# Kernel optimization log

Measured on AMD Instinct MI355X. Metric: run time of the kernel, lower is better.

Reference implementation:

```python
import jax, jax.numpy as jnp
import numpy as np

TAU = 0.5
EPS = 1e-6
RAY_STEPS = 128
N_SECANT = 8
STEPS_IN = 64
STEPS_OUT = 32
RADIUS = 1.0
ADA_START, ADA_END, ADA_DECAY = 2.0, 0.1, 1.5e-5
IT = 100000
DEPTH_NEAR = 0.0
DELTA = float(max(ADA_START * np.exp(-ADA_DECAY * IT), ADA_END))


def _occ_val(p, W1, b1, W2, b2):
    # occupancy probability minus tau (sign change = surface crossing)
    h = jax.nn.softplus(p @ W1 + b1)
    return jax.nn.sigmoid((h @ W2 + b2)[..., 0]) - TAU


def _rgb_alpha(p, v, W1, b1, W2, b2, Wc1, bc1, Wc2, bc2):
    alpha = _occ_val(p, W1, b1, W2, b2) + TAU
    f = jax.nn.relu(jnp.concatenate([p, v], -1) @ Wc1 + bc1)
    rgb = jax.nn.sigmoid(f @ Wc2 + bc2)
    return rgb, alpha


def _forward(pixels, camera_mat, world_mat, scale_mat, W1, b1, W2, b2, Wc1, bc1, Wc2, bc2):
    B, N, _ = pixels.shape
    # transform_to_world with all matrices inverted: p_world = S^-1 W^-1 C^-1 p_hom
    M = jnp.linalg.inv(scale_mat) @ jnp.linalg.inv(world_mat) @ jnp.linalg.inv(camera_mat)
    ones = jnp.ones((B, N, 1), pixels.dtype)
    p_h = jnp.concatenate([pixels, ones, ones], -1)  # (x, y, 1, 1) with depth 1
    pixels_world = jnp.einsum('bij,bnj->bni', M, p_h)[..., :3]
    origin = jnp.array([0.0, 0.0, 0.0, 1.0], pixels.dtype)
    cam0 = jnp.einsum('bij,j->bi', M, origin)[..., :3]                 # (B,3)
    camera_world = jnp.broadcast_to(cam0[:, None, :], (B, N, 3))
    ray = pixels_world - camera_world
    ray = ray / jnp.linalg.norm(ray, axis=-1, keepdims=True)

    # ---- sphere intersection ----
    rcd = jnp.einsum('bnd,bd->bn', ray, cam0)
    under = rcd ** 2 - (jnp.sum(cam0 ** 2, -1)[:, None] - RADIUS ** 2)
    mask_int = under > 0
    s = jnp.sqrt(jnp.where(mask_int, under, 1.0))                      # safe sqrt
    inters = jnp.stack([-s - rcd, s - rcd], -1)
    inters = jnp.where(mask_int[..., None], inters, 0.0)
    inters = jnp.maximum(inters, 0.0)                                  # (B,N,2)
    d_far = inters[..., 1]

    # ---- ray marching + secant root finding (no grad in original) ----
    t = jnp.linspace(0.0, 1.0, RAY_STEPS, dtype=pixels.dtype)
    d_prop = d_far[..., None] * t                                      # (B,N,S)
    p_prop = camera_world[:, :, None, :] + ray[:, :, None, :] * d_prop[..., None]
    val = _occ_val(p_prop, W1, b1, W2, b2)                             # (B,N,S)
    mask_0_free = val[..., 0] < 0
    sign = jnp.sign(val[..., :-1] * val[..., 1:])
    sign = jnp.concatenate([sign, jnp.ones_like(sign[..., :1])], -1)
    cost = sign * jnp.arange(RAY_STEPS, 0, -1, dtype=pixels.dtype)
    ind = jnp.argmin(cost, -1)
    mask_sc = jnp.min(cost, -1) < 0
    f_low = jnp.take_along_axis(val, ind[..., None], -1)[..., 0]
    mask = mask_sc & (f_low < 0) & mask_int & mask_0_free
    ind_hi = jnp.minimum(ind + 1, RAY_STEPS - 1)
    d_low = jnp.take_along_axis(d_prop, ind[..., None], -1)[..., 0]
    d_high = jnp.take_along_axis(d_prop, ind_hi[..., None], -1)[..., 0]
    f_high = jnp.take_along_axis(val, ind_hi[..., None], -1)[..., 0]

    def sec(f_l, f_h, d_l, d_h):
        den = f_h - f_l
        return jnp.where(jnp.abs(den) > 1e-12, -f_l * (d_h - d_l) / den + d_l, 0.5 * (d_l + d_h))

    def body(i, c):
        d_p, d_l, f_l, d_h, f_h = c
        f_m = _occ_val(camera_world + ray * d_p[..., None], W1, b1, W2, b2)
        low = f_m < 0
        d_l = jnp.where(low, d_p, d_l); f_l = jnp.where(low, f_m, f_l)
        d_h = jnp.where(low, d_h, d_p); f_h = jnp.where(low, f_h, f_m)
        return (sec(f_l, f_h, d_l, d_h), d_l, f_l, d_h, f_h)

    d_pred0 = sec(f_low, f_high, d_low, d_high)
    d_pred, _, _, _, _ = jax.lax.fori_loop(0, N_SECANT, body, (d_pred0, d_low, f_low, d_high, f_high))
    d_i = jnp.where(mask, d_pred, jnp.inf)
    d_i = jnp.where(mask_0_free, d_i, 0.0)
    d_i = jax.lax.stop_gradient(d_i)

    # ---- depth interval selection ----
    mask_zero = d_i == 0
    mask_pred = jnp.isfinite(d_i)
    dists = jnp.where(mask_pred, d_i, 1.0)
    dists = jnp.where(mask_zero, 0.0, dists)[0]                        # batch 1, as original
    obj_mask = (mask_pred & ~mask_zero)[0]                             # (N,)
    cam_f = camera_world.reshape(-1, 3)
    ray_f = ray.reshape(-1, 3)
    d_surf = inters.reshape(-1, 2)[:, 1]
    dnp = jnp.maximum(dists - DELTA, DEPTH_NEAR)
    dfp = jnp.minimum(dists + DELTA, d_surf)
    FULL = STEPS_IN + STEPS_OUT
    t_full = jnp.linspace(0.0, 1.0, FULL, dtype=pixels.dtype)
    d_bg = d_surf[:, None] * t_full                                    # depth_range[0] = 0
    t_in = jnp.linspace(0.0, 1.0, STEPS_IN, dtype=pixels.dtype)
    t_out = jnp.linspace(0.0, 1.0, STEPS_OUT, dtype=pixels.dtype)
    d_in = dnp[:, None] * (1.0 - t_in) + dfp[:, None] * t_in
    d_out = dnp[:, None] * t_out
    d_obj = jnp.sort(jnp.concatenate([d_out, d_in], -1), -1)
    d_all = jnp.where(obj_mask[:, None], d_obj, d_bg)                  # (N, FULL)

    # ---- shading + alpha compositing ----
    p_fg = cam_f[:, None, :] + ray_f[:, None, :] * d_all[..., None]    # (N,FULL,3)
    v_fg = jnp.broadcast_to(-ray_f[:, None, :], p_fg.shape)
    rgb, alpha = _rgb_alpha(p_fg, v_fg, W1, b1, W2, b2, Wc1, bc1, Wc2, bc2)
    trans = jnp.cumprod(jnp.concatenate([jnp.ones_like(alpha[:, :1]), 1.0 - alpha + EPS], -1), -1)[:, :-1]
    w = alpha * trans
    rgb_values = jnp.sum(w[..., None] * rgb, -2)
    return rgb_values.reshape(B, N, 3)


def setup_inputs() -> dict:
    key = jax.random.key(0)
    ks = jax.random.split(key, 8)
    B, N, H = 1, 4096, 128
    pixels = jax.random.uniform(ks[0], (B, N, 2), minval=-1.0, maxval=1.0, dtype=jnp.float32)
    camera_mat = jnp.broadcast_to(jnp.diag(jnp.array([2.0, 2.0, 1.0, 1.0], jnp.float32)), (B, 4, 4))
    world_mat = jnp.broadcast_to(jnp.array([[1, 0, 0, 0], [0, 1, 0, 0], [0, 0, 1, 2.0], [0, 0, 0, 1]], jnp.float32), (B, 4, 4))
    scale_mat = jnp.broadcast_to(jnp.eye(4, dtype=jnp.float32), (B, 4, 4))
    W1 = jax.random.normal(ks[1], (3, H), jnp.float32)
    b1 = 0.1 * jax.random.normal(ks[2], (H,), jnp.float32)
    W2 = 0.5 * jax.random.normal(ks[3], (H, 1), jnp.float32)
    b2 = jnp.zeros((1,), jnp.float32)
    Wc1 = 0.5 * jax.random.normal(ks[4], (6, H), jnp.float32)
    bc1 = jnp.zeros((H,), jnp.float32)
    Wc2 = 0.5 * jax.random.normal(ks[5], (H, 3), jnp.float32)
    bc2 = jnp.zeros((3,), jnp.float32)
    return dict(pixels=pixels, camera_mat=camera_mat, world_mat=world_mat, scale_mat=scale_mat,
                W1=W1, b1=b1, W2=W2, b2=b2, Wc1=Wc1, bc1=bc1, Wc2=Wc2, bc2=bc2)


def reference(pixels, camera_mat, world_mat, scale_mat, W1, b1, W2, b2, Wc1, bc1, Wc2, bc2):
    return _forward(pixels, camera_mat, world_mat, scale_mat, W1, b1, W2, b2, Wc1, bc1, Wc2, bc2)
```

## Files before the change

kernel.cpp:

```cpp
#include <hip/hip_runtime.h>
#include <math.h>


namespace {

constexpr int H_    = 128;
constexpr int RS    = 128;
constexpr int NSEC  = 8;
constexpr int SOUT_ = 32;
constexpr int SIN_  = 64;
constexpr int FULL_ = 96;
constexpr float EPSA   = 1e-6f;
constexpr float DELTA_ = 0.44626032029685964f;
constexpr float L2E    = 1.4426950408889634f;
constexpr float LN2    = 0.6931471805599453f;

typedef __attribute__((ext_vector_type(2))) float f2;

__device__ __forceinline__ f2 s2(float v) { return f2{v, v}; }

constexpr float PC0 =  0.5849625007211562f;
constexpr float PC1 =  0.4808983469629878f;
constexpr float PC2 = -0.0801497244938313f;
constexpr float PC3 =  0.0178110498875181f;
constexpr float PC4 = -0.0044527624718795f;
constexpr float PC5 =  0.0011873633258345f;
constexpr float PC6 = -0.0003298231460651f;

__device__ __forceinline__ f2 sp2p(f2 u) {
    f2 e;
    e.x = __builtin_amdgcn_exp2f(-fabsf(u.x));
    e.y = __builtin_amdgcn_exp2f(-fabsf(u.y));
    f2 t = e + e - 1.0f;
    f2 p = s2(PC6);
    p = __builtin_elementwise_fma(p, t, s2(PC5));
    p = __builtin_elementwise_fma(p, t, s2(PC4));
    p = __builtin_elementwise_fma(p, t, s2(PC3));
    p = __builtin_elementwise_fma(p, t, s2(PC2));
    p = __builtin_elementwise_fma(p, t, s2(PC1));
    p = __builtin_elementwise_fma(p, t, s2(PC0));
    return __builtin_elementwise_max(u, s2(0.0f)) + p;
}

__device__ __forceinline__ float sigmoid_fast(float x) {
    return __builtin_amdgcn_rcpf(1.0f + __expf(-x));
}
__device__ __forceinline__ float sgnf(float p) {
    return (p > 0.0f) ? 1.0f : ((p < 0.0f) ? -1.0f : 0.0f);
}
__device__ __forceinline__ float secant_step(float f_l, float f_h, float d_l, float d_h) {
    float den = f_h - f_l;
    if (fabsf(den) > 1e-12f) return -f_l * (d_h - d_l) / den + d_l;
    return 0.5f * (d_l + d_h);
}

__device__ void inv4(const float* m, float* o) {
    float inv[16];
    inv[0]  =  m[5]*m[10]*m[15] - m[5]*m[11]*m[14] - m[9]*m[6]*m[15] + m[9]*m[7]*m[14] + m[13]*m[6]*m[11] - m[13]*m[7]*m[10];
    inv[4]  = -m[4]*m[10]*m[15] + m[4]*m[11]*m[14] + m[8]*m[6]*m[15] - m[8]*m[7]*m[14] - m[12]*m[6]*m[11] + m[12]*m[7]*m[10];
    inv[8]  =  m[4]*m[9]*m[15]  - m[4]*m[11]*m[13] - m[8]*m[5]*m[15] + m[8]*m[7]*m[13] + m[12]*m[5]*m[11] - m[12]*m[7]*m[9];
    inv[12] = -m[4]*m[9]*m[14]  + m[4]*m[10]*m[13] + m[8]*m[5]*m[14] - m[8]*m[6]*m[13] - m[12]*m[5]*m[10] + m[12]*m[6]*m[9];
    inv[1]  = -m[1]*m[10]*m[15] + m[1]*m[11]*m[14] + m[9]*m[2]*m[15] - m[9]*m[3]*m[14] - m[13]*m[2]*m[11] + m[13]*m[3]*m[10];
    inv[5]  =  m[0]*m[10]*m[15] - m[0]*m[11]*m[14] - m[8]*m[2]*m[15] + m[8]*m[3]*m[14] + m[12]*m[2]*m[11] - m[12]*m[3]*m[10];
    inv[9]  = -m[0]*m[9]*m[15]  + m[0]*m[11]*m[13] + m[8]*m[1]*m[15] - m[8]*m[3]*m[13] - m[12]*m[1]*m[11] + m[12]*m[3]*m[9];
    inv[13] =  m[0]*m[9]*m[14]  - m[0]*m[10]*m[13] - m[8]*m[1]*m[14] + m[8]*m[2]*m[13] + m[12]*m[1]*m[10] - m[12]*m[2]*m[9];
    inv[2]  =  m[1]*m[6]*m[15]  - m[1]*m[7]*m[14]  - m[5]*m[2]*m[15] + m[5]*m[3]*m[14] + m[13]*m[2]*m[7]  - m[13]*m[3]*m[6];
    inv[6]  = -m[0]*m[6]*m[15]  + m[0]*m[7]*m[14]  + m[4]*m[2]*m[15] - m[4]*m[3]*m[14] - m[12]*m[2]*m[7]  + m[12]*m[3]*m[6];
    inv[10] =  m[0]*m[5]*m[15]  - m[0]*m[7]*m[13]  - m[4]*m[1]*m[15] + m[4]*m[3]*m[13] + m[12]*m[1]*m[7]  - m[12]*m[3]*m[5];
    inv[14] = -m[0]*m[5]*m[14]  + m[0]*m[6]*m[13]  + m[4]*m[1]*m[14] - m[4]*m[2]*m[13] - m[12]*m[1]*m[6]  + m[12]*m[2]*m[5];
    inv[3]  = -m[1]*m[6]*m[11]  + m[1]*m[7]*m[10]  + m[5]*m[2]*m[11] - m[5]*m[3]*m[10] - m[9]*m[2]*m[7]   + m[9]*m[3]*m[6];
    inv[7]  =  m[0]*m[6]*m[11]  - m[0]*m[7]*m[10]  - m[4]*m[2]*m[11] + m[4]*m[3]*m[10] + m[8]*m[2]*m[7]   - m[8]*m[3]*m[6];
    inv[11] = -m[0]*m[5]*m[11]  + m[0]*m[7]*m[9]   + m[4]*m[1]*m[11] - m[4]*m[3]*m[9]  - m[8]*m[1]*m[7]   + m[8]*m[3]*m[5];
    inv[15] =  m[0]*m[5]*m[10]  - m[0]*m[6]*m[9]   - m[4]*m[1]*m[10] + m[4]*m[2]*m[9]  + m[8]*m[1]*m[6]   - m[8]*m[2]*m[5];
    float det = m[0]*inv[0] + m[1]*inv[4] + m[2]*inv[8] + m[3]*inv[12];
    float idet = 1.0f / det;
    for (int i = 0; i < 16; i++) o[i] = inv[i] * idet;
}

__global__ __launch_bounds__(64) void render_k(
    const float* __restrict__ pixels,
    const float* __restrict__ Cm, const float* __restrict__ Wm, const float* __restrict__ Sm,
    const float* __restrict__ W1, const float* __restrict__ b1,
    const float* __restrict__ W2, const float* __restrict__ b2,
    const float* __restrict__ Wc1, const float* __restrict__ bc1,
    const float* __restrict__ Wc2, const float* __restrict__ bc2,
    float* __restrict__ out, int N)
{
    const int tid = threadIdx.x;
    const int r   = blockIdx.x;

    __shared__ float4 sP0[H_/2];
    __shared__ float4 sP1[H_/2];
    __shared__ float4 sP2[H_/2];
    __shared__ float4 sP3[H_/2];
    __shared__ f2     sW2[H_/2];
    __shared__ float  sInv[3][16];
    __shared__ float  sT[16], sM[16];

    {
        const float* mm = (tid == 0) ? Cm : ((tid == 1) ? Wm : Sm);
        float o[16];
        inv4(mm, o);
        if (tid < 3)
            for (int k = 0; k < 16; k++) sInv[tid][k] = o[k];
    }
    __syncthreads();
    if (tid < 16) {
        int row = tid >> 2, col = tid & 3;
        float s = 0.0f;
        for (int k = 0; k < 4; k++) s += sInv[1][row*4 + k] * sInv[0][k*4 + col];
        sT[tid] = s;
    }
    __syncthreads();
    if (tid < 16) {
        int row = tid >> 2, col = tid & 3;
        float s = 0.0f;
        for (int k = 0; k < 4; k++) s += sInv[2][row*4 + k] * sT[k*4 + col];
        sM[tid] = s;
    }
    __syncthreads();

    float cx, cy, cz, rx, ry, rz, dfar;
    int mint;
    {
        const float px_ = pixels[2*r], py_ = pixels[2*r + 1];
        float cam[3], dir[3];
        for (int i = 0; i < 3; i++) {
            cam[i] = sM[4*i + 3];
            float pw = sM[4*i + 0]*px_ + sM[4*i + 1]*py_ + sM[4*i + 2] + sM[4*i + 3];
            dir[i] = pw - cam[i];
        }
        float nrm = sqrtf(dir[0]*dir[0] + dir[1]*dir[1] + dir[2]*dir[2]);
        rx = dir[0]/nrm; ry = dir[1]/nrm; rz = dir[2]/nrm;
        cx = cam[0]; cy = cam[1]; cz = cam[2];
        float rcd = rx*cx + ry*cy + rz*cz;
        float cc  = cx*cx + cy*cy + cz*cz;
        float under = rcd*rcd - (cc - 1.0f);
        mint = under > 0.0f;
        float s = sqrtf(mint ? under : 1.0f);
        dfar = mint ? fmaxf(s - rcd, 0.0f) : 0.0f;
    }

    float a2k[2], c2k[2], w2k[2];
    float cCr[2], w0r[2], w1r[2], w2r[2];
#pragma unroll
    for (int k = 0; k < 2; k++) {
        const int u = 2*tid + k;
        float w1x = W1[u], w1y = W1[H_ + u], w1z = W1[2*H_ + u];
        float b1j = b1[u], w2j = W2[u];
        a2k[k] = (w1x*rx + w1y*ry + w1z*rz) * L2E;
        c2k[k] = (w1x*cx + w1y*cy + w1z*cz + b1j) * L2E;
        w2k[k] = w2j * LN2;
        float q0 = Wc1[u],        q1 = Wc1[H_ + u],  q2 = Wc1[2*H_ + u];
        float q3 = Wc1[3*H_ + u], q4 = Wc1[4*H_ + u], q5 = Wc1[5*H_ + u];
        float aC = q0*rx + q1*ry + q2*rz;
        cCr[k] = q0*cx + q1*cy + q2*cz + bc1[u] - (q3*rx + q4*ry + q5*rz);
        w0r[k] = Wc2[3*u + 0]; w1r[k] = Wc2[3*u + 1]; w2r[k] = Wc2[3*u + 2];
        if (k == 0) {
            sP0[tid].x = a2k[0]; sP0[tid].z = c2k[0];
            sP1[tid].x = w2k[0]; sP1[tid].z = aC;
            sP2[tid].x = cCr[0]; sP2[tid].z = w0r[0];
            sP3[tid].x = w1r[0]; sP3[tid].z = w2r[0];
        } else {
            sP0[tid].y = a2k[1]; sP0[tid].w = c2k[1];
            sP1[tid].y = w2k[1]; sP1[tid].w = aC;
            sP2[tid].y = cCr[1]; sP2[tid].w = w0r[1];
            sP3[tid].y = w1r[1]; sP3[tid].w = w2r[1];
        }
    }
    sW2[tid] = f2{w2k[0], w2k[1]};
    const float b2v  = b2[0];
    const float bc20 = bc2[0], bc21 = bc2[1], bc22 = bc2[2];
    __syncthreads();

    float alpha0, r0c, g0c, b0c;
    float alpha1, r1c, g1c, b1c;

    if (dfar == 0.0f) {
        f2 sp = sp2p(f2{c2k[0], c2k[1]});
        float part = sp.x*w2k[0] + sp.y*w2k[1];
        f2 ff = __builtin_elementwise_max(f2{cCr[0], cCr[1]}, s2(0.0f));
        float A0 = ff.x*w0r[0] + ff.y*w0r[1];
        float A1 = ff.x*w1r[0] + ff.y*w1r[1];
        float A2 = ff.x*w2r[0] + ff.y*w2r[1];
#pragma unroll
        for (int off = 32; off; off >>= 1) {
            part += __shfl_xor(part, off, 64);
            A0   += __shfl_xor(A0,   off, 64);
            A1   += __shfl_xor(A1,   off, 64);
            A2   += __shfl_xor(A2,   off, 64);
        }
        alpha0 = sigmoid_fast(part + b2v);
        r0c = sigmoid_fast(A0 + bc20);
        g0c = sigmoid_fast(A1 + bc21);
        b0c = sigmoid_fast(A2 + bc22);
        alpha1 = alpha0; r1c = r0c; g1c = g0c; b1c = b0c;
    } else {
        const float inv127 = 1.0f / (RS - 1);

        float l0;
        {
            f2 sp = sp2p(f2{c2k[0], c2k[1]});
            float part = sp.x*w2k[0] + sp.y*w2k[1];
#pragma unroll
            for (int off = 32; off; off >>= 1) part += __shfl_xor(part, off, 64);
            l0 = part + b2v;
        }

        float d_i;
        if (l0 >= 0.0f) {
            d_i = 0.0f;
        } else {
            auto march_logit = [&](float dsmp) -> float {
                const f2 dd = s2(dsmp);
                f2 acc = s2(0.0f);
#pragma unroll 4
                for (int j2 = 0; j2 < H_/2; j2++) {
                    float4 q0 = sP0[j2];
                    f2 wv = sW2[j2];
                    f2 u = __builtin_elementwise_fma(f2{q0.x, q0.y}, dd, f2{q0.z, q0.w});
                    acc = __builtin_elementwise_fma(sp2p(u), wv, acc);
                }
                return acc.x + acc.y + b2v;
            };

            float lA = march_logit(dfar * ((float)tid * inv127));
            float va = sigmoid_fast(lA) - 0.5f;
            float van = __shfl_down(va, 1, 64);
            float ca = (tid < 63) ? sgnf(va * van) * (float)(RS - tid) : 1.0f;
            float cmin = ca; int ind = tid;
#pragma unroll
            for (int off = 32; off; off >>= 1) {
                float c2 = __shfl_xor(cmin, off, 64);
                int   i2 = __shfl_xor(ind,  off, 64);
                if (c2 < cmin || (c2 == cmin && i2 < ind)) { cmin = c2; ind = i2; }
            }
            int crossed = cmin < 0.0f;
            float f_low = 0.0f, f_high = 0.0f;
            if (crossed) {
                f_low  = __shfl(va, ind, 64);
                f_high = __shfl(va, ind + 1, 64);
            } else {
                float lB = march_logit(dfar * ((float)(tid + 64) * inv127));
                float vb = sigmoid_fast(lB) - 0.5f;
                float v63 = __shfl(va, 63, 64);
                float v64 = __shfl(vb, 0, 64);
                if (v63 * v64 < 0.0f) {
                    crossed = 1; ind = 63;
                    f_low = v63; f_high = v64;
                } else {
                    float vbn = __shfl_down(vb, 1, 64);
                    float cb = (tid < 63) ? sgnf(vb * vbn) * (float)(64 - tid) : 1.0f;
                    float cminb = cb; int indl = tid;
#pragma unroll
                    for (int off = 32; off; off >>= 1) {
                        float c2 = __shfl_xor(cminb, off, 64);
                        int   i2 = __shfl_xor(indl,  off, 64);
                        if (c2 < cminb || (c2 == cminb && i2 < indl)) { cminb = c2; indl = i2; }
                    }
                    if (cminb < 0.0f) {
                        crossed = 1; ind = 64 + indl;
                        f_low  = __shfl(vb, indl, 64);
                        f_high = __shfl(vb, indl + 1, 64);
                    }
                }
            }

            const int msk = crossed && (f_low < 0.0f) && mint;
            if (msk) {
                float d_l = dfar * ((float)ind * inv127);
                float d_h = dfar * ((float)(ind + 1) * inv127);
                float f_l = f_low, f_h = f_high;
                float d_p = secant_step(f_l, f_h, d_l, d_h);
                for (int it = 0; it < NSEC; it++) {
                    f2 u2 = __builtin_elementwise_fma(f2{a2k[0], a2k[1]}, s2(d_p),
                                                      f2{c2k[0], c2k[1]});
                    f2 sp = sp2p(u2);
                    float part = sp.x*w2k[0] + sp.y*w2k[1];
#pragma unroll
                    for (int off = 32; off; off >>= 1) part += __shfl_xor(part, off, 64);
                    float fm = sigmoid_fast(part + b2v) - 0.5f;
                    bool low = fm < 0.0f;
                    d_l = low ? d_p : d_l;  f_l = low ? fm : f_l;
                    d_h = low ? d_h : d_p;  f_h = low ? f_h : fm;
                    d_p = secant_step(f_l, f_h, d_l, d_h);
                }
                d_i = d_p;
            } else {
                d_i = INFINITY;
            }
        }

        const int mask_zero = (d_i == 0.0f);
        const int mask_pred = isfinite(d_i);
        float dists = mask_pred ? d_i : 1.0f;
        if (mask_zero) dists = 0.0f;
        const int obj = mask_pred && !mask_zero;
        const float dnp = fmaxf(dists - DELTA_, 0.0f);
        const float dfp = fminf(dists + DELTA_, dfar);

        auto sample_d = [&](int s) -> float {
            if (obj) {
                if (s < SOUT_) return dnp * ((float)s * (1.0f / (SOUT_ - 1)));
                float u = (float)(s - SOUT_) * (1.0f / (SIN_ - 1));
                return dnp * (1.0f - u) + dfp * u;
            }
            return dfar * ((float)s * (1.0f / (FULL_ - 1)));
        };

        {
            const f2 dd = s2(sample_d(tid));
            f2 SO = s2(0.0f), A0 = s2(0.0f), A1 = s2(0.0f), A2 = s2(0.0f);
#pragma unroll 4
            for (int j2 = 0; j2 < H_/2; j2++) {
                float4 q0 = sP0[j2];
                float4 q1 = sP1[j2];
                float4 q2 = sP2[j2];
                float4 q3 = sP3[j2];
                f2 u = __builtin_elementwise_fma(f2{q0.x, q0.y}, dd, f2{q0.z, q0.w});
                SO = __builtin_elementwise_fma(sp2p(u), f2{q1.x, q1.y}, SO);
                f2 f = __builtin_elementwise_max(
                           __builtin_elementwise_fma(f2{q1.z, q1.w}, dd, f2{q2.x, q2.y}),
                           s2(0.0f));
                A0 = __builtin_elementwise_fma(f, f2{q2.z, q2.w}, A0);
                A1 = __builtin_elementwise_fma(f, f2{q3.x, q3.y}, A1);
                A2 = __builtin_elementwise_fma(f, f2{q3.z, q3.w}, A2);
            }
            alpha0 = sigmoid_fast(SO.x + SO.y + b2v);
            r0c = sigmoid_fast(A0.x + A0.y + bc20);
            g0c = sigmoid_fast(A1.x + A1.y + bc21);
            b0c = sigmoid_fast(A2.x + A2.y + bc22);
        }

        {
            const int s1 = 64 + (tid & 31);
            const int jb = (tid >> 5) * (H_/4);
            const f2 dd = s2(sample_d(s1));
            f2 SO = s2(0.0f), A0 = s2(0.0f), A1 = s2(0.0f), A2 = s2(0.0f);
#pragma unroll 4
            for (int j2 = jb; j2 < jb + H_/4; j2++) {
                float4 q0 = sP0[j2];
                float4 q1 = sP1[j2];
                float4 q2 = sP2[j2];
                float4 q3 = sP3[j2];
                f2 u = __builtin_elementwise_fma(f2{q0.x, q0.y}, dd, f2{q0.z, q0.w});
                SO = __builtin_elementwise_fma(sp2p(u), f2{q1.x, q1.y}, SO);
                f2 f = __builtin_elementwise_max(
                           __builtin_elementwise_fma(f2{q1.z, q1.w}, dd, f2{q2.x, q2.y}),
                           s2(0.0f));
                A0 = __builtin_elementwise_fma(f, f2{q2.z, q2.w}, A0);
                A1 = __builtin_elementwise_fma(f, f2{q3.x, q3.y}, A1);
                A2 = __builtin_elementwise_fma(f, f2{q3.z, q3.w}, A2);
            }
            float SOs = SO.x + SO.y, A0s = A0.x + A0.y;
            float A1s = A1.x + A1.y, A2s = A2.x + A2.y;
            SOs += __shfl_xor(SOs, 32, 64);
            A0s += __shfl_xor(A0s, 32, 64);
            A1s += __shfl_xor(A1s, 32, 64);
            A2s += __shfl_xor(A2s, 32, 64);
            alpha1 = sigmoid_fast(SOs + b2v);
            r1c = sigmoid_fast(A0s + bc20);
            g1c = sigmoid_fast(A1s + bc21);
            b1c = sigmoid_fast(A2s + bc22);
        }
    }

    {
        float mA = 1.0f - alpha0 + EPSA;
        float p = mA;
#pragma unroll
        for (int off = 1; off < 64; off <<= 1) {
            float v = __shfl_up(p, off, 64);
            if (tid >= off) p *= v;
        }
        float TexA = __shfl_up(p, 1, 64);
        if (tid == 0) TexA = 1.0f;
        float TA = __shfl(p, 63, 64);
        float wA = alpha0 * TexA;

        float mB = (tid < 32) ? (1.0f - alpha1 + EPSA) : 1.0f;
        float pb = mB;
#pragma unroll
        for (int off = 1; off < 32; off <<= 1) {
            float v = __shfl_up(pb, off, 64);
            if (tid >= off) pb *= v;
        }
        float TexB = __shfl_up(pb, 1, 64);
        if (tid == 0) TexB = 1.0f;
        float wB = (tid < 32) ? alpha1 * TexB * TA : 0.0f;

        float s0 = wA*r0c + wB*r1c;
        float s1 = wA*g0c + wB*g1c;
        float s2v = wA*b0c + wB*b1c;
#pragma unroll
        for (int off = 32; off; off >>= 1) {
            s0  += __shfl_xor(s0,  off, 64);
            s1  += __shfl_xor(s1,  off, 64);
            s2v += __shfl_xor(s2v, off, 64);
        }
        if (tid == 0) {
            out[3*r + 0] = s0;
            out[3*r + 1] = s1;
            out[3*r + 2] = s2v;
        }
    }
}

}

extern "C" void kernel_launch(void* const* d_in, const int* in_sizes, int n_in,
                              void* d_out, int out_size, void* d_ws, size_t ws_size,
                              hipStream_t stream) {
    const float* pixels = (const float*)d_in[0];
    const float* Cm  = (const float*)d_in[1];
    const float* Wm  = (const float*)d_in[2];
    const float* Sm  = (const float*)d_in[3];
    const float* W1  = (const float*)d_in[4];
    const float* b1  = (const float*)d_in[5];
    const float* W2  = (const float*)d_in[6];
    const float* b2  = (const float*)d_in[7];
    const float* Wc1 = (const float*)d_in[8];
    const float* bc1 = (const float*)d_in[9];
    const float* Wc2 = (const float*)d_in[10];
    const float* bc2 = (const float*)d_in[11];
    float* out = (float*)d_out;

    const int N = in_sizes[0] / 2;
    hipLaunchKernelGGL(render_k, dim3(N), dim3(64), 0, stream,
                       pixels, Cm, Wm, Sm, W1, b1, W2, b2, Wc1, bc1, Wc2, bc2, out, N);
}
```

Measured before the change: 98.60 us.

## Pack four rays per block, one wavefront each, with vectorized weight loads

Each block now handles four rays, one per 64-lane wavefront, with per-wave shared-memory parameter tables. The 4x4 matrix inversion and the launch overhead are shared across four rays instead of being repeated for every ray. Weight loads become float2 vector loads issued before the first barrier, and the shared tables are written as whole float4 values. The cost is more shared memory per block and block-wide syncs that couple the four waves, plus a clamp and guard for tail rays.

```diff
diff --git a/kernel.cpp b/kernel.cpp
--- a/kernel.cpp
+++ b/kernel.cpp
@@ -10,6 +10,7 @@
 constexpr int SOUT_ = 32;
 constexpr int SIN_  = 64;
 constexpr int FULL_ = 96;
+constexpr int RPB   = 4;
 constexpr float EPSA   = 1e-6f;
 constexpr float DELTA_ = 0.44626032029685964f;
 constexpr float L2E    = 1.4426950408889634f;
@@ -52,6 +53,9 @@
     float den = f_h - f_l;
     if (fabsf(den) > 1e-12f) return -f_l * (d_h - d_l) / den + d_l;
     return 0.5f * (d_l + d_h);
+}
+__device__ __forceinline__ float2 ld2(const float* p) {
+    return *reinterpret_cast<const float2*>(p);
 }
 
 __device__ void inv4(const float* m, float* o) {
@@ -77,7 +81,7 @@
     for (int i = 0; i < 16; i++) o[i] = inv[i] * idet;
 }
 
-__global__ __launch_bounds__(64) void render_k(
+__global__ __launch_bounds__(64 * RPB) void render_k(
     const float* __restrict__ pixels,
     const float* __restrict__ Cm, const float* __restrict__ Wm, const float* __restrict__ Sm,
     const float* __restrict__ W1, const float* __restrict__ b1,
@@ -86,44 +90,66 @@
     const float* __restrict__ Wc2, const float* __restrict__ bc2,
     float* __restrict__ out, int N)
 {
-    const int tid = threadIdx.x;
-    const int r   = blockIdx.x;
-
-    __shared__ float4 sP0[H_/2];
-    __shared__ float4 sP1[H_/2];
-    __shared__ float4 sP2[H_/2];
-    __shared__ float4 sP3[H_/2];
-    __shared__ f2     sW2[H_/2];
+    const int tid  = threadIdx.x;
+    const int lane = tid & 63;
+    const int wid  = tid >> 6;
+    const int r    = blockIdx.x * RPB + wid;
+    const int rr   = (r < N) ? r : (N - 1);
+
+    __shared__ float4 sP0[RPB][H_/2];
+    __shared__ float4 sP1[RPB][H_/2];
+    __shared__ float4 sP2[RPB][H_/2];
+    __shared__ float4 sP3[RPB][H_/2];
+    __shared__ f2     sW2[RPB][H_/2];
     __shared__ float  sInv[3][16];
     __shared__ float  sT[16], sM[16];
 
-    {
-        const float* mm = (tid == 0) ? Cm : ((tid == 1) ? Wm : Sm);
+    const int u0 = 2 * lane;
+    const float2 w1xv = ld2(W1 + u0);
+    const float2 w1yv = ld2(W1 + H_ + u0);
+    const float2 w1zv = ld2(W1 + 2*H_ + u0);
+    const float2 b1v  = ld2(b1 + u0);
+    const float2 w2v  = ld2(W2 + u0);
+    const float2 q0v  = ld2(Wc1 + u0);
+    const float2 q1v  = ld2(Wc1 + H_ + u0);
+    const float2 q2v  = ld2(Wc1 + 2*H_ + u0);
+    const float2 q3v  = ld2(Wc1 + 3*H_ + u0);
+    const float2 q4v  = ld2(Wc1 + 4*H_ + u0);
+    const float2 q5v  = ld2(Wc1 + 5*H_ + u0);
+    const float2 bc1v = ld2(bc1 + u0);
+    const float2 wc2a = ld2(Wc2 + 3*u0);
+    const float2 wc2b = ld2(Wc2 + 3*u0 + 2);
+    const float2 wc2c = ld2(Wc2 + 3*u0 + 4);
+    const float b2v  = b2[0];
+    const float bc20 = bc2[0], bc21 = bc2[1], bc22 = bc2[2];
+
+    if (wid == 0) {
+        const float* mm = (lane == 0) ? Cm : ((lane == 1) ? Wm : Sm);
         float o[16];
         inv4(mm, o);
-        if (tid < 3)
-            for (int k = 0; k < 16; k++) sInv[tid][k] = o[k];
+        if (lane < 3)
+            for (int k = 0; k < 16; k++) sInv[lane][k] = o[k];
     }
     __syncthreads();
-    if (tid < 16) {
-        int row = tid >> 2, col = tid & 3;
+    if (wid == 0 && lane < 16) {
+        int row = lane >> 2, col = lane & 3;
         float s = 0.0f;
         for (int k = 0; k < 4; k++) s += sInv[1][row*4 + k] * sInv[0][k*4 + col];
-        sT[tid] = s;
+        sT[lane] = s;
     }
     __syncthreads();
-    if (tid < 16) {
-        int row = tid >> 2, col = tid & 3;
+    if (wid == 0 && lane < 16) {
+        int row = lane >> 2, col = lane & 3;
         float s = 0.0f;
         for (int k = 0; k < 4; k++) s += sInv[2][row*4 + k] * sT[k*4 + col];
-        sM[tid] = s;
+        sM[lane] = s;
     }
     __syncthreads();
 
     float cx, cy, cz, rx, ry, rz, dfar;
     int mint;
     {
-        const float px_ = pixels[2*r], py_ = pixels[2*r + 1];
+        const float px_ = pixels[2*rr], py_ = pixels[2*rr + 1];
         float cam[3], dir[3];
         for (int i = 0; i < 3; i++) {
             cam[i] = sM[4*i + 3];
@@ -143,34 +169,25 @@
 
     float a2k[2], c2k[2], w2k[2];
     float cCr[2], w0r[2], w1r[2], w2r[2];
-#pragma unroll
-    for (int k = 0; k < 2; k++) {
-        const int u = 2*tid + k;
-        float w1x = W1[u], w1y = W1[H_ + u], w1z = W1[2*H_ + u];
-        float b1j = b1[u], w2j = W2[u];
-        a2k[k] = (w1x*rx + w1y*ry + w1z*rz) * L2E;
-        c2k[k] = (w1x*cx + w1y*cy + w1z*cz + b1j) * L2E;
-        w2k[k] = w2j * LN2;
-        float q0 = Wc1[u],        q1 = Wc1[H_ + u],  q2 = Wc1[2*H_ + u];
-        float q3 = Wc1[3*H_ + u], q4 = Wc1[4*H_ + u], q5 = Wc1[5*H_ + u];
-        float aC = q0*rx + q1*ry + q2*rz;
-        cCr[k] = q0*cx + q1*cy + q2*cz + bc1[u] - (q3*rx + q4*ry + q5*rz);
-        w0r[k] = Wc2[3*u + 0]; w1r[k] = Wc2[3*u + 1]; w2r[k] = Wc2[3*u + 2];
-        if (k == 0) {
-            sP0[tid].x = a2k[0]; sP0[tid].z = c2k[0];
-            sP1[tid].x = w2k[0]; sP1[tid].z = aC;
-            sP2[tid].x = cCr[0]; sP2[tid].z = w0r[0];
-            sP3[tid].x = w1r[0]; sP3[tid].z = w2r[0];
-        } else {
-            sP0[tid].y = a2k[1]; sP0[tid].w = c2k[1];
-            sP1[tid].y = w2k[1]; sP1[tid].w = aC;
-            sP2[tid].y = cCr[1]; sP2[tid].w = w0r[1];
-            sP3[tid].y = w1r[1]; sP3[tid].w = w2r[1];
-        }
-    }
-    sW2[tid] = f2{w2k[0], w2k[1]};
-    const float b2v  = b2[0];
-    const float bc20 = bc2[0], bc21 = bc2[1], bc22 = bc2[2];
+    {
+        a2k[0] = (w1xv.x*rx + w1yv.x*ry + w1zv.x*rz) * L2E;
+        a2k[1] = (w1xv.y*rx + w1yv.y*ry + w1zv.y*rz) * L2E;
+        c2k[0] = (w1xv.x*cx + w1yv.x*cy + w1zv.x*cz + b1v.x) * L2E;
+        c2k[1] = (w1xv.y*cx + w1yv.y*cy + w1zv.y*cz + b1v.y) * L2E;
+        w2k[0] = w2v.x * LN2;
+        w2k[1] = w2v.y * LN2;
+        float aC0 = q0v.x*rx + q1v.x*ry + q2v.x*rz;
+        float aC1 = q0v.y*rx + q1v.y*ry + q2v.y*rz;
+        cCr[0] = q0v.x*cx + q1v.x*cy + q2v.x*cz + bc1v.x - (q3v.x*rx + q4v.x*ry + q5v.x*rz);
+        cCr[1] = q0v.y*cx + q1v.y*cy + q2v.y*cz + bc1v.y - (q3v.y*rx + q4v.y*ry + q5v.y*rz);
+        w0r[0] = wc2a.x; w1r[0] = wc2a.y; w2r[0] = wc2b.x;
+        w0r[1] = wc2b.y; w1r[1] = wc2c.x; w2r[1] = wc2c.y;
+        sP0[wid][lane] = float4{a2k[0], a2k[1], c2k[0], c2k[1]};
+        sP1[wid][lane] = float4{w2k[0], w2k[1], aC0, aC1};
+        sP2[wid][lane] = float4{cCr[0], cCr[1], w0r[0], w0r[1]};
+        sP3[wid][lane] = float4{w1r[0], w1r[1], w2r[0], w2r[1]};
+        sW2[wid][lane] = f2{w2k[0], w2k[1]};
+    }
     __syncthreads();
 
     float alpha0, r0c, g0c, b0c;
@@ -216,19 +233,19 @@
                 f2 acc = s2(0.0f);
 #pragma unroll 4
                 for (int j2 = 0; j2 < H_/2; j2++) {
-                    float4 q0 = sP0[j2];
-                    f2 wv = sW2[j2];
+                    float4 q0 = sP0[wid][j2];
+                    f2 wv = sW2[wid][j2];
                     f2 u = __builtin_elementwise_fma(f2{q0.x, q0.y}, dd, f2{q0.z, q0.w});
                     acc = __builtin_elementwise_fma(sp2p(u), wv, acc);
                 }
                 return acc.x + acc.y + b2v;
             };
 
-            float lA = march_logit(dfar * ((float)tid * inv127));
+            float lA = march_logit(dfar * ((float)lane * inv127));
             float va = sigmoid_fast(lA) - 0.5f;
             float van = __shfl_down(va, 1, 64);
-            float ca = (tid < 63) ? sgnf(va * van) * (float)(RS - tid) : 1.0f;
-            float cmin = ca; int ind = tid;
+            float ca = (lane < 63) ? sgnf(va * van) * (float)(RS - lane) : 1.0f;
+            float cmin = ca; int ind = lane;
 #pragma unroll
             for (int off = 32; off; off >>= 1) {
                 float c2 = __shfl_xor(cmin, off, 64);
@@ -241,7 +258,7 @@
                 f_low  = __shfl(va, ind, 64);
                 f_high = __shfl(va, ind + 1, 64);
             } else {
-                float lB = march_logit(dfar * ((float)(tid + 64) * inv127));
+                float lB = march_logit(dfar * ((float)(lane + 64) * inv127));
                 float vb = sigmoid_fast(lB) - 0.5f;
                 float v63 = __shfl(va, 63, 64);
                 float v64 = __shfl(vb, 0, 64);
@@ -250,8 +267,8 @@
                     f_low = v63; f_high = v64;
                 } else {
                     float vbn = __shfl_down(vb, 1, 64);
-                    float cb = (tid < 63) ? sgnf(vb * vbn) * (float)(64 - tid) : 1.0f;
-                    float cminb = cb; int indl = tid;
+                    float cb = (lane < 63) ? sgnf(vb * vbn) * (float)(64 - lane) : 1.0f;
+                    float cminb = cb; int indl = lane;
 #pragma unroll
                     for (int off = 32; off; off >>= 1) {
                         float c2 = __shfl_xor(cminb, off, 64);
@@ -309,14 +326,14 @@
         };
 
         {
-            const f2 dd = s2(sample_d(tid));
+            const f2 dd = s2(sample_d(lane));
             f2 SO = s2(0.0f), A0 = s2(0.0f), A1 = s2(0.0f), A2 = s2(0.0f);
 #pragma unroll 4
             for (int j2 = 0; j2 < H_/2; j2++) {
-                float4 q0 = sP0[j2];
-                float4 q1 = sP1[j2];
-                float4 q2 = sP2[j2];
-                float4 q3 = sP3[j2];
+                float4 q0 = sP0[wid][j2];
+                float4 q1 = sP1[wid][j2];
+                float4 q2 = sP2[wid][j2];
+                float4 q3 = sP3[wid][j2];
                 f2 u = __builtin_elementwise_fma(f2{q0.x, q0.y}, dd, f2{q0.z, q0.w});
                 SO = __builtin_elementwise_fma(sp2p(u), f2{q1.x, q1.y}, SO);
                 f2 f = __builtin_elementwise_max(
@@ -333,16 +350,16 @@
         }
 
         {
-            const int s1 = 64 + (tid & 31);
-            const int jb = (tid >> 5) * (H_/4);
+            const int s1 = 64 + (lane & 31);
+            const int jb = (lane >> 5) * (H_/4);
             const f2 dd = s2(sample_d(s1));
             f2 SO = s2(0.0f), A0 = s2(0.0f), A1 = s2(0.0f), A2 = s2(0.0f);
 #pragma unroll 4
             for (int j2 = jb; j2 < jb + H_/4; j2++) {
-                float4 q0 = sP0[j2];
-                float4 q1 = sP1[j2];
-                float4 q2 = sP2[j2];
-                float4 q3 = sP3[j2];
+                float4 q0 = sP0[wid][j2];
+                float4 q1 = sP1[wid][j2];
+                float4 q2 = sP2[wid][j2];
+                float4 q3 = sP3[wid][j2];
                 f2 u = __builtin_elementwise_fma(f2{q0.x, q0.y}, dd, f2{q0.z, q0.w});
                 SO = __builtin_elementwise_fma(sp2p(u), f2{q1.x, q1.y}, SO);
                 f2 f = __builtin_elementwise_max(
@@ -371,23 +388,23 @@
 #pragma unroll
         for (int off = 1; off < 64; off <<= 1) {
             float v = __shfl_up(p, off, 64);
-            if (tid >= off) p *= v;
+            if (lane >= off) p *= v;
         }
         float TexA = __shfl_up(p, 1, 64);
-        if (tid == 0) TexA = 1.0f;
+        if (lane == 0) TexA = 1.0f;
         float TA = __shfl(p, 63, 64);
         float wA = alpha0 * TexA;
 
-        float mB = (tid < 32) ? (1.0f - alpha1 + EPSA) : 1.0f;
+        float mB = (lane < 32) ? (1.0f - alpha1 + EPSA) : 1.0f;
         float pb = mB;
 #pragma unroll
         for (int off = 1; off < 32; off <<= 1) {
             float v = __shfl_up(pb, off, 64);
-            if (tid >= off) pb *= v;
+            if (lane >= off) pb *= v;
         }
         float TexB = __shfl_up(pb, 1, 64);
-        if (tid == 0) TexB = 1.0f;
-        float wB = (tid < 32) ? alpha1 * TexB * TA : 0.0f;
+        if (lane == 0) TexB = 1.0f;
+        float wB = (lane < 32) ? alpha1 * TexB * TA : 0.0f;
 
         float s0 = wA*r0c + wB*r1c;
         float s1 = wA*g0c + wB*g1c;
@@ -398,7 +415,7 @@
             s1  += __shfl_xor(s1,  off, 64);
             s2v += __shfl_xor(s2v, off, 64);
         }
-        if (tid == 0) {
+        if (lane == 0 && r < N) {
             out[3*r + 0] = s0;
             out[3*r + 1] = s1;
             out[3*r + 2] = s2v;
@@ -426,6 +443,7 @@
     float* out = (float*)d_out;
 
     const int N = in_sizes[0] / 2;
-    hipLaunchKernelGGL(render_k, dim3(N), dim3(64), 0, stream,
+    const int nblk = (N + RPB - 1) / RPB;
+    hipLaunchKernelGGL(render_k, dim3(nblk), dim3(64 * RPB), 0, stream,
                        pixels, Cm, Wm, Sm, W1, b1, W2, b2, Wc1, bc1, Wc2, bc2, out, N);
 }
```

Measured after the change: 98.98 us. About the same (+0.4%).
